# Performance work log

Measured on AMD Instinct MI355X. Metric: run time of the kernel, lower is better.

The kernel has to match this reference:

```python
import jax, jax.numpy as jnp
import numpy as np
import math
from jax import lax

SQRT_HALF = math.sqrt(0.5)

def _causal_dilated_conv(x, w, b, dilation):
    # x: [B, C, T], w: [O, I, K] (torch layout), causal left padding (K-1)*dilation
    k = w.shape[-1]
    pad = (k - 1) * dilation
    y = lax.conv_general_dilated(
        x, w,
        window_strides=(1,),
        padding=((pad, 0),),
        rhs_dilation=(dilation,),
        dimension_numbers=('NCH', 'OIH', 'NCH'),
    )
    return y + b[None, :, None]


def setup_inputs() -> dict:
    key = jax.random.key(0)
    ks = jax.random.split(key, 9)
    B, C, S, T, K = 8, 512, 256, 8192, 2
    scale = 1.0 / np.sqrt(C * K)
    return {
        'x': jax.random.normal(ks[0], (B, C, T), jnp.float32),
        'filter_w': jax.random.normal(ks[1], (C, C, K), jnp.float32) * scale,
        'filter_b': jax.random.normal(ks[2], (C,), jnp.float32) * scale,
        'gate_w': jax.random.normal(ks[3], (C, C, K), jnp.float32) * scale,
        'gate_b': jax.random.normal(ks[4], (C,), jnp.float32) * scale,
        'res_w': jax.random.normal(ks[5], (C, C), jnp.float32) / np.sqrt(C),
        'res_b': jax.random.normal(ks[6], (C,), jnp.float32) / np.sqrt(C),
        'skip_w': jax.random.normal(ks[7], (S, C), jnp.float32) / np.sqrt(C),
        'skip_b': jax.random.normal(ks[8], (S,), jnp.float32) / np.sqrt(C),
        'dilation': 4,
    }


def reference(x, filter_w, filter_b, gate_w, gate_b, res_w, res_b, skip_w, skip_b, dilation):
    filter_out = jnp.tanh(_causal_dilated_conv(x, filter_w, filter_b, dilation))
    gate_out = jax.nn.sigmoid(_causal_dilated_conv(x, gate_w, gate_b, dilation))
    x_gated = filter_out * gate_out  # [B, C, T]
    # 1x1 convs as channel contractions
    res_out = jnp.einsum('oc,bct->bot', res_w, x_gated) + res_b[None, :, None]
    skip_out = jnp.einsum('sc,bct->bst', skip_w, x_gated) + skip_b[None, :, None]
    return ((x + res_out) * SQRT_HALF, skip_out)
```

## Files before the change

### kernel.cpp

```cpp
#include <hip/hip_runtime.h>
#include <hip/hip_bf16.h>

typedef __attribute__((ext_vector_type(4))) float f32x4;
typedef __attribute__((ext_vector_type(8))) short bf16x8;
typedef unsigned int   u32;
typedef unsigned short u16;

#define DPAD 8
#define B_   8
#define C_   512
#define T_   8192
#define S_   256

#define OFF_WBIG 0u
#define OFF_W2   2097152u
#define OFF_B1   2883584u
#define OFF_B2   2887680u
#define OFF_XT   2891776u
#define OFF_ZT   70066176u

__device__ __forceinline__ u16 f2bf(float f) {
  u32 u = __builtin_bit_cast(u32, f);
  u += 0x7FFFu + ((u >> 16) & 1u);
  return (u16)(u >> 16);
}
__device__ __forceinline__ float sigm_(float x) { return 1.0f / (1.0f + __expf(-x)); }
__device__ __forceinline__ float tanh_(float x) { return 2.0f / (1.0f + __expf(-2.0f * x)) - 1.0f; }

__device__ __forceinline__ void gload_lds16(const void* g, void* l) {
  __builtin_amdgcn_global_load_lds(
      (const __attribute__((address_space(1))) void*)g,
      (__attribute__((address_space(3))) void*)l, 16, 0, 0);
}

__global__ void pack_kernel(const float* __restrict__ fw, const float* __restrict__ fb,
                            const float* __restrict__ gw, const float* __restrict__ gb,
                            const float* __restrict__ rw, const float* __restrict__ rb,
                            const float* __restrict__ sw, const float* __restrict__ sb,
                            u16* __restrict__ Wbig, u16* __restrict__ W2,
                            float* __restrict__ b1, float* __restrict__ b2,
                            u16* __restrict__ Xt)
{
  int idx = blockIdx.x * 256 + threadIdx.x;
  if (idx < 1048576) {
    int row = idx >> 10, k = idx & 1023;
    int i = row >> 1;
    const float* src = (row & 1) ? gw : fw;
    float v = src[((i << 9) + (k & 511)) * 2 + ((k < 512) ? 1 : 0)];
    Wbig[idx] = f2bf(v);
    return;
  }
  idx -= 1048576;
  if (idx < 393216) {
    int r = idx >> 9, k = idx & 511;
    float v = (r < 512) ? rw[(r << 9) + k] : sw[((r - 512) << 9) + k];
    W2[idx] = f2bf(v);
    return;
  }
  idx -= 393216;
  if (idx < 1024) { b1[idx] = (idx & 1) ? gb[idx >> 1] : fb[idx >> 1]; return; }
  idx -= 1024;
  if (idx < 768) { b2[idx] = (idx < 512) ? rb[idx] : sb[idx - 512]; return; }
  idx -= 768;
  if (idx < B_ * DPAD * C_) {
    int b = idx >> 12;
    int rest = idx & 4095;
    Xt[(size_t)b * (T_ + DPAD) * C_ + rest] = 0;
  }
}

__global__ __launch_bounds__(256) void transpose_kernel(const float* __restrict__ x,
                                                        u16* __restrict__ Xt)
{
  __shared__ float tile[64][65];
  int bid = blockIdx.x;
  int ct = bid & 7, tt = (bid >> 3) & 127, b = bid >> 10;
  int w = threadIdx.x >> 6, ln = threadIdx.x & 63;
  const float* xp = x + ((size_t)(b * C_ + ct * 64)) * T_ + tt * 64;
#pragma unroll
  for (int r = 0; r < 16; ++r) {
    int cl = r * 4 + w;
    tile[cl][ln] = xp[(size_t)cl * T_ + ln];
  }
  __syncthreads();
  u16* op = Xt + ((size_t)b * (T_ + DPAD) + DPAD + tt * 64) * C_ + ct * 64;
#pragma unroll
  for (int r = 0; r < 16; ++r) {
    int tl = r * 4 + w;
    op[(size_t)tl * C_ + ln] = f2bf(tile[ln][tl]);
  }
}

__global__ __launch_bounds__(512, 2) void gemm1_kernel(
    const u16* __restrict__ W, const u16* __restrict__ Xt,
    const float* __restrict__ b1, u16* __restrict__ Zt,
    const int* __restrict__ dptr)
{
  __shared__ __align__(16) u16 smem[4 * 16384];
  const int dcap = *dptr;
  const int tid = threadIdx.x;
  const int lane = tid & 63, wave = tid >> 6;
  const int wm = wave >> 2, wn = wave & 3;

  const int bid = blockIdx.x;
  const int xcd = bid & 7;
  const int idx = bid >> 3;
  const int mt  = idx & 3;
  const int nt  = (xcd << 5) | (idx >> 2);
  const int m0  = mt * 256;
  const int n0g = nt * 256;
  const int b = n0g >> 13, t0 = n0g & (T_ - 1);

  const int row0 = tid >> 3;
  const int ksw  = (((tid & 7) ^ (row0 & 7)) << 3);
  const size_t xtb = (size_t)b * (T_ + DPAD) * C_;

  f32x4 acc[8][4];
#pragma unroll
  for (int i = 0; i < 8; ++i)
#pragma unroll
    for (int j = 0; j < 4; ++j) acc[i][j] = (f32x4){0.f, 0.f, 0.f, 0.f};

#define STAGE1(kt_, dd) do {                                                   \
    const int kglob_ = (kt_) * 64 + ksw;                                       \
    const int col_ = kglob_ & 511;                                             \
    const int rsh_ = (kglob_ >= 512) ? dcap : 0;                               \
    const u16* gA_ = W + (size_t)(m0 + row0) * 1024 + kglob_;                  \
    const u16* gB_ = Xt + xtb + (size_t)(DPAD + t0 + row0 - rsh_) * C_ + col_; \
    u16* As_ = smem + (dd) * 16384;                                            \
    u16* Bs_ = smem + 32768 + (dd) * 16384;                                    \
    _Pragma("unroll") for (int r_ = 0; r_ < 4; ++r_) {                         \
      gload_lds16(gA_ + (size_t)r_ * 64 * 1024, As_ + r_ * 4096 + tid * 8);    \
      gload_lds16(gB_ + (size_t)r_ * 64 * C_,   Bs_ + r_ * 4096 + tid * 8);    \
    }                                                                          \
  } while (0)

#define COMPUTE1(dd) do {                                                      \
    const u16* Ab_ = smem + (dd) * 16384;                                      \
    const u16* Bb_ = smem + 32768 + (dd) * 16384;                              \
    _Pragma("unroll") for (int s_ = 0; s_ < 2; ++s_) {                         \
      const int blk_ = ((s_ * 4 + (lane >> 4)) ^ (lane & 7)) * 8;              \
      bf16x8 af_[8], bf_[4];                                                   \
      _Pragma("unroll") for (int i_ = 0; i_ < 8; ++i_)                         \
        af_[i_] = *(const bf16x8*)(Ab_ + (wm * 128 + i_ * 16 + (lane & 15)) * 64 + blk_); \
      _Pragma("unroll") for (int j_ = 0; j_ < 4; ++j_)                         \
        bf_[j_] = *(const bf16x8*)(Bb_ + (wn * 64 + j_ * 16 + (lane & 15)) * 64 + blk_);  \
      __builtin_amdgcn_s_setprio(1);                                           \
      _Pragma("unroll") for (int i_ = 0; i_ < 8; ++i_)                         \
        _Pragma("unroll") for (int j_ = 0; j_ < 4; ++j_)                       \
          acc[i_][j_] = __builtin_amdgcn_mfma_f32_16x16x32_bf16(af_[i_], bf_[j_], acc[i_][j_], 0, 0, 0); \
      __builtin_amdgcn_s_setprio(0);                                           \
    }                                                                          \
  } while (0)

  STAGE1(0, 0);
  STAGE1(1, 1);
  for (int it = 0; it < 15; ++it) {
    asm volatile("s_waitcnt vmcnt(8)" ::: "memory");
    __builtin_amdgcn_sched_barrier(0);
    __builtin_amdgcn_s_barrier();
    __builtin_amdgcn_sched_barrier(0);
    COMPUTE1(it & 1);
    __builtin_amdgcn_sched_barrier(0);
    __builtin_amdgcn_s_barrier();
    __builtin_amdgcn_sched_barrier(0);
    if (it < 14) STAGE1(it + 2, it & 1);
  }
  asm volatile("s_waitcnt vmcnt(0)" ::: "memory");
  __builtin_amdgcn_sched_barrier(0);
  __builtin_amdgcn_s_barrier();
  __builtin_amdgcn_sched_barrier(0);
  COMPUTE1(1);

  const int g = lane >> 4, p = lane & 15;
#pragma unroll
  for (int i = 0; i < 8; ++i) {
    const int R = m0 + wm * 128 + i * 16 + (g << 2);
    const float bi0 = b1[R], bi1 = b1[R + 1], bi2 = b1[R + 2], bi3 = b1[R + 3];
    const int c0 = R >> 1;
#pragma unroll
    for (int j = 0; j < 4; ++j) {
      const int ttc = t0 + wn * 64 + j * 16 + p;
      f32x4 v = acc[i][j];
      float z0 = tanh_(v[0] + bi0) * sigm_(v[1] + bi1);
      float z1 = tanh_(v[2] + bi2) * sigm_(v[3] + bi3);
      u32 pk = (u32)f2bf(z0) | ((u32)f2bf(z1) << 16);
      *(u32*)(Zt + (size_t)(b * T_ + ttc) * C_ + c0) = pk;
    }
  }
#undef STAGE1
#undef COMPUTE1
}

__global__ __launch_bounds__(256, 4) void gemm2_kernel(
    const u16* __restrict__ W2, const u16* __restrict__ Zt,
    const float* __restrict__ b2, const float* __restrict__ x,
    float* __restrict__ out)
{
  __shared__ __align__(16) u16 As[128 * 32];
  __shared__ __align__(16) u16 Bs[128 * 32];
  __shared__ __align__(16) float fstall[4 * 1088];
  const int tid = threadIdx.x;
  const int lane = tid & 63, wave = tid >> 6;
  const int wm = wave >> 1, wn = wave & 1;

  const int bid = blockIdx.x;
  const int xcd = bid & 7;
  const int idx = bid >> 3;
  const int mt  = idx % 6;
  const int nt  = (xcd << 6) + idx / 6;
  const int m0 = mt * 128;
  const int n0g = nt * 128;
  const int b = n0g >> 13, t0 = n0g & (T_ - 1);
  const int srow = tid >> 2;
  const int skk  = (tid & 3) * 8;

  f32x4 acc[4][4];
#pragma unroll
  for (int i = 0; i < 4; ++i)
#pragma unroll
    for (int j = 0; j < 4; ++j) acc[i][j] = (f32x4){0.f, 0.f, 0.f, 0.f};

  const int aoff = (wm * 64 + (lane & 15)) * 32 + (lane >> 4) * 8;
  const int boff = (wn * 64 + (lane & 15)) * 32 + (lane >> 4) * 8;
  const size_t ztb = (size_t)b * T_ * C_;

  for (int kc = 0; kc < 16; ++kc) {
    const int k = kc * 32 + skk;
    const u16* gA = W2 + (size_t)(m0 + srow) * 512 + k;
    const u16* gB = Zt + ztb + (size_t)(t0 + srow) * C_ + k;
    gload_lds16(gA,            As + tid * 8);
    gload_lds16(gA + 64 * 512, As + 2048 + tid * 8);
    gload_lds16(gB,            Bs + tid * 8);
    gload_lds16(gB + 64 * C_,  Bs + 2048 + tid * 8);
    asm volatile("s_waitcnt vmcnt(0)" ::: "memory");
    __syncthreads();
    bf16x8 af[4], bfr[4];
#pragma unroll
    for (int i = 0; i < 4; ++i) af[i]  = *(const bf16x8*)(As + aoff + i * 512);
#pragma unroll
    for (int j = 0; j < 4; ++j) bfr[j] = *(const bf16x8*)(Bs + boff + j * 512);
#pragma unroll
    for (int i = 0; i < 4; ++i)
#pragma unroll
      for (int j = 0; j < 4; ++j)
        acc[i][j] = __builtin_amdgcn_mfma_f32_16x16x32_bf16(af[i], bfr[j], acc[i][j], 0, 0, 0);
    __syncthreads();
  }

  float* const fst = fstall + wave * 1088;
  const int g = lane >> 4, p = lane & 15;
  const bool isres = (m0 < 512);

#pragma unroll
  for (int i = 0; i < 4; ++i) {
#pragma unroll
    for (int j = 0; j < 4; ++j)
#pragma unroll
      for (int r = 0; r < 4; ++r)
        fst[(g * 4 + r) * 68 + j * 16 + p] = acc[i][j][r];
#pragma unroll
    for (int q = 0; q < 4; ++q) {
      const int lrow = q * 4 + g;
      const int row = m0 + wm * 64 + i * 16 + lrow;
      const int t = t0 + wn * 64 + p * 4;
      f32x4 v = *(const f32x4*)&fst[lrow * 68 + p * 4];
      const float bias = b2[row];
      f32x4 res;
      if (isres) {
        const size_t o = ((size_t)(b * 512 + row)) * T_ + t;
        f32x4 xv = *(const f32x4*)(x + o);
#pragma unroll
        for (int e = 0; e < 4; ++e)
          res[e] = (xv[e] + v[e] + bias) * 0.70710678118654752f;
        *(f32x4*)(out + o) = res;
      } else {
        const size_t o = (size_t)33554432 + ((size_t)(b * 256 + (row - 512))) * T_ + t;
#pragma unroll
        for (int e = 0; e < 4; ++e)
          res[e] = v[e] + bias;
        *(f32x4*)(out + o) = res;
      }
    }
  }
}

extern "C" void kernel_launch(void* const* d_in, const int* in_sizes, int n_in,
                              void* d_out, int out_size, void* d_ws, size_t ws_size,
                              hipStream_t stream) {
  const float* x  = (const float*)d_in[0];
  const float* fw = (const float*)d_in[1];
  const float* fb = (const float*)d_in[2];
  const float* gw = (const float*)d_in[3];
  const float* gb = (const float*)d_in[4];
  const float* rw = (const float*)d_in[5];
  const float* rb = (const float*)d_in[6];
  const float* sw = (const float*)d_in[7];
  const float* sb = (const float*)d_in[8];
  const int* dil  = (const int*)d_in[9];

  char* ws = (char*)d_ws;
  u16*   Wbig = (u16*)(ws + OFF_WBIG);
  u16*   W2   = (u16*)(ws + OFF_W2);
  float* b1   = (float*)(ws + OFF_B1);
  float* b2   = (float*)(ws + OFF_B2);
  u16*   Xt   = (u16*)(ws + OFF_XT);
  u16*   Zt   = (u16*)(ws + OFF_ZT);
  float* out  = (float*)d_out;

  hipLaunchKernelGGL(pack_kernel, dim3(5767), dim3(256), 0, stream,
                     fw, fb, gw, gb, rw, rb, sw, sb, Wbig, W2, b1, b2, Xt);
  hipLaunchKernelGGL(transpose_kernel, dim3(8192), dim3(256), 0, stream, x, Xt);
  hipLaunchKernelGGL(gemm1_kernel, dim3(1024), dim3(512), 0, stream, Wbig, Xt, b1, Zt, dil);
  hipLaunchKernelGGL(gemm2_kernel, dim3(3072), dim3(256), 0, stream, W2, Zt, b2, x, out);
}
```

Baseline: 317.3 us.

## Split gemm1 main loop into four phases interleaving loads with MFMA

Restructures the gemm1 K-loop from a two-stage-ahead prefetch with two barriers per tile into four phases per tile. Each phase issues a slice of the next tile's global-to-LDS loads alongside a slice of MFMA work, with B fragments held in registers across phases. The aim is to spread memory issue across compute and keep the matrix units fed. In exchange the prefetch depth drops from two tiles to one and there are more barriers, which may expose load latency.

Measured after the change: 307.4 us. 1.03x faster.

```diff
diff --git a/kernel.cpp b/kernel.cpp
--- a/kernel.cpp
+++ b/kernel.cpp
@@ -96,11 +96,12 @@
     const float* __restrict__ b1, u16* __restrict__ Zt,
     const int* __restrict__ dptr)
 {
-  __shared__ __align__(16) u16 smem[4 * 16384];
+  __shared__ __align__(16) u16 smem[65536];
   const int dcap = *dptr;
   const int tid = threadIdx.x;
   const int lane = tid & 63, wave = tid >> 6;
   const int wm = wave >> 2, wn = wave & 3;
+  const int lp = lane & 15, lg = lane >> 4, lx = lane & 7;
 
   const int bid = blockIdx.x;
   const int xcd = bid & 7;
@@ -110,67 +111,80 @@
   const int m0  = mt * 256;
   const int n0g = nt * 256;
   const int b = n0g >> 13, t0 = n0g & (T_ - 1);
-
-  const int row0 = tid >> 3;
-  const int ksw  = (((tid & 7) ^ (row0 & 7)) << 3);
   const size_t xtb = (size_t)b * (T_ + DPAD) * C_;
 
+  const int srl = tid >> 3;
+  const int skb = tid & 7;
+  const int sxk = (skb ^ (srl & 7)) << 3;
+
   f32x4 acc[8][4];
 #pragma unroll
   for (int i = 0; i < 8; ++i)
 #pragma unroll
     for (int j = 0; j < 4; ++j) acc[i][j] = (f32x4){0.f, 0.f, 0.f, 0.f};
 
-#define STAGE1(kt_, dd) do {                                                   \
-    const int kglob_ = (kt_) * 64 + ksw;                                       \
-    const int col_ = kglob_ & 511;                                             \
-    const int rsh_ = (kglob_ >= 512) ? dcap : 0;                               \
-    const u16* gA_ = W + (size_t)(m0 + row0) * 1024 + kglob_;                  \
-    const u16* gB_ = Xt + xtb + (size_t)(DPAD + t0 + row0 - rsh_) * C_ + col_; \
-    u16* As_ = smem + (dd) * 16384;                                            \
-    u16* Bs_ = smem + 32768 + (dd) * 16384;                                    \
-    _Pragma("unroll") for (int r_ = 0; r_ < 4; ++r_) {                         \
-      gload_lds16(gA_ + (size_t)r_ * 64 * 1024, As_ + r_ * 4096 + tid * 8);    \
-      gload_lds16(gB_ + (size_t)r_ * 64 * C_,   Bs_ + r_ * 4096 + tid * 8);    \
-    }                                                                          \
+#define SQA(kt_, dd, q_) do {                                                  \
+    const int row_ = (q_) * 64 + srl;                                          \
+    gload_lds16(W + (size_t)(m0 + row_) * 1024 + (kt_) * 64 + sxk,             \
+                smem + (dd) * 16384 + (q_) * 4096 + tid * 8);                  \
   } while (0)
 
-#define COMPUTE1(dd) do {                                                      \
+#define SQB(kt_, dd, q_) do {                                                  \
+    const int row_ = (q_) * 64 + srl;                                          \
+    const int kg_  = (kt_) * 64 + sxk;                                         \
+    const int rsh_ = (kg_ >= 512) ? dcap : 0;                                  \
+    gload_lds16(Xt + xtb + (size_t)(DPAD + t0 + row_ - rsh_) * C_ + (kg_ & 511), \
+                smem + 32768 + (dd) * 16384 + (q_) * 4096 + tid * 8);          \
+  } while (0)
+
+#define LDA_(Ab_, f_, kk_) \
+  (*(const bf16x8*)((Ab_) + (size_t)(wm * 128 + (f_) * 16 + lp) * 64 + ((((kk_) * 4 + lg) ^ lx) << 3)))
+#define LDB_(Bb_, j_, kk_) \
+  (*(const bf16x8*)((Bb_) + (size_t)(wn * 64 + (j_) * 16 + lp) * 64 + ((((kk_) * 4 + lg) ^ lx) << 3)))
+
+#define PH(dd, p_, WAITS, STAGES) do {                                         \
+    WAITS;                                                                     \
+    __builtin_amdgcn_sched_barrier(0);                                         \
+    __builtin_amdgcn_s_barrier();                                              \
+    __builtin_amdgcn_sched_barrier(0);                                         \
     const u16* Ab_ = smem + (dd) * 16384;                                      \
     const u16* Bb_ = smem + 32768 + (dd) * 16384;                              \
-    _Pragma("unroll") for (int s_ = 0; s_ < 2; ++s_) {                         \
-      const int blk_ = ((s_ * 4 + (lane >> 4)) ^ (lane & 7)) * 8;              \
-      bf16x8 af_[8], bf_[4];                                                   \
-      _Pragma("unroll") for (int i_ = 0; i_ < 8; ++i_)                         \
-        af_[i_] = *(const bf16x8*)(Ab_ + (wm * 128 + i_ * 16 + (lane & 15)) * 64 + blk_); \
-      _Pragma("unroll") for (int j_ = 0; j_ < 4; ++j_)                         \
-        bf_[j_] = *(const bf16x8*)(Bb_ + (wn * 64 + j_ * 16 + (lane & 15)) * 64 + blk_);  \
-      __builtin_amdgcn_s_setprio(1);                                           \
-      _Pragma("unroll") for (int i_ = 0; i_ < 8; ++i_)                         \
-        _Pragma("unroll") for (int j_ = 0; j_ < 4; ++j_)                       \
-          acc[i_][j_] = __builtin_amdgcn_mfma_f32_16x16x32_bf16(af_[i_], bf_[j_], acc[i_][j_], 0, 0, 0); \
-      __builtin_amdgcn_s_setprio(0);                                           \
+    if ((p_) == 0) {                                                           \
+      _Pragma("unroll") for (int j_ = 0; j_ < 4; ++j_) {                       \
+        bfr[j_][0] = LDB_(Bb_, j_, 0); bfr[j_][1] = LDB_(Bb_, j_, 1);          \
+      }                                                                        \
     }                                                                          \
+    bf16x8 a00 = LDA_(Ab_, 2 * (p_), 0),     a01 = LDA_(Ab_, 2 * (p_), 1);     \
+    bf16x8 a10 = LDA_(Ab_, 2 * (p_) + 1, 0), a11 = LDA_(Ab_, 2 * (p_) + 1, 1); \
+    STAGES;                                                                    \
+    __builtin_amdgcn_s_setprio(1);                                             \
+    _Pragma("unroll") for (int j_ = 0; j_ < 4; ++j_) {                         \
+      acc[2*(p_)][j_]   = __builtin_amdgcn_mfma_f32_16x16x32_bf16(a00, bfr[j_][0], acc[2*(p_)][j_],   0, 0, 0); \
+      acc[2*(p_)][j_]   = __builtin_amdgcn_mfma_f32_16x16x32_bf16(a01, bfr[j_][1], acc[2*(p_)][j_],   0, 0, 0); \
+      acc[2*(p_)+1][j_] = __builtin_amdgcn_mfma_f32_16x16x32_bf16(a10, bfr[j_][0], acc[2*(p_)+1][j_], 0, 0, 0); \
+      acc[2*(p_)+1][j_] = __builtin_amdgcn_mfma_f32_16x16x32_bf16(a11, bfr[j_][1], acc[2*(p_)+1][j_], 0, 0, 0); \
+    }                                                                          \
+    __builtin_amdgcn_s_setprio(0);                                             \
   } while (0)
 
-  STAGE1(0, 0);
-  STAGE1(1, 1);
-  for (int it = 0; it < 15; ++it) {
-    asm volatile("s_waitcnt vmcnt(8)" ::: "memory");
-    __builtin_amdgcn_sched_barrier(0);
-    __builtin_amdgcn_s_barrier();
-    __builtin_amdgcn_sched_barrier(0);
-    COMPUTE1(it & 1);
-    __builtin_amdgcn_sched_barrier(0);
-    __builtin_amdgcn_s_barrier();
-    __builtin_amdgcn_sched_barrier(0);
-    if (it < 14) STAGE1(it + 2, it & 1);
-  }
-  asm volatile("s_waitcnt vmcnt(0)" ::: "memory");
-  __builtin_amdgcn_sched_barrier(0);
-  __builtin_amdgcn_s_barrier();
-  __builtin_amdgcn_sched_barrier(0);
-  COMPUTE1(1);
+#define VMW(n_) asm volatile("s_waitcnt vmcnt(" #n_ ")" ::: "memory")
+
+  bf16x8 bfr[4][2];
+
+  SQB(0, 0, 0); SQB(0, 0, 1); SQB(0, 0, 2); SQB(0, 0, 3);
+  SQA(0, 0, 0); SQA(0, 0, 2); SQA(0, 0, 1); SQA(0, 0, 3);
+
+  for (int t = 0; t < 15; ++t) {
+    const int dd = t & 1, de = dd ^ 1;
+    PH(dd, 0, VMW(2), { SQB(t + 1, de, 0); SQB(t + 1, de, 1); });
+    PH(dd, 1,       , { SQB(t + 1, de, 2); SQB(t + 1, de, 3); });
+    PH(dd, 2, VMW(4), { SQA(t + 1, de, 0); SQA(t + 1, de, 2); });
+    PH(dd, 3,       , { SQA(t + 1, de, 1); SQA(t + 1, de, 3); });
+  }
+  PH(1, 0, VMW(2), );
+  PH(1, 1,       , );
+  PH(1, 2, VMW(0), );
+  PH(1, 3,       , );
 
   const int g = lane >> 4, p = lane & 15;
 #pragma unroll
@@ -188,8 +202,12 @@
       *(u32*)(Zt + (size_t)(b * T_ + ttc) * C_ + c0) = pk;
     }
   }
-#undef STAGE1
-#undef COMPUTE1
+#undef SQA
+#undef SQB
+#undef LDA_
+#undef LDB_
+#undef PH
+#undef VMW
 }
 
 __global__ __launch_bounds__(256, 4) void gemm2_kernel(
```

## Replace LDS-staged gemm1 mainloop with direct global-to-register double-buffered loads

Applied to the files above, without the earlier changes.

The gemm1 kernel no longer stages A and B tiles through shared memory with async global-to-LDS loads and barriers. Each wave now loads its MFMA fragments directly from global memory into registers, double-buffered across 32-wide k steps. This removes the LDS traffic and workgroup barriers. In exchange, tiles shared across waves are fetched redundantly from global or L2, loads are less coalesced, and register pressure rises, which can hurt occupancy.

Result: slower. 544.5 us (+71.6%).

```diff
diff --git a/kernel.cpp b/kernel.cpp
--- a/kernel.cpp
+++ b/kernel.cpp
@@ -96,11 +96,11 @@
     const float* __restrict__ b1, u16* __restrict__ Zt,
     const int* __restrict__ dptr)
 {
-  __shared__ __align__(16) u16 smem[4 * 16384];
   const int dcap = *dptr;
   const int tid = threadIdx.x;
   const int lane = tid & 63, wave = tid >> 6;
   const int wm = wave >> 2, wn = wave & 3;
+  const int lp = lane & 15, lg = lane >> 4;
 
   const int bid = blockIdx.x;
   const int xcd = bid & 7;
@@ -110,9 +110,6 @@
   const int m0  = mt * 256;
   const int n0g = nt * 256;
   const int b = n0g >> 13, t0 = n0g & (T_ - 1);
-
-  const int row0 = tid >> 3;
-  const int ksw  = (((tid & 7) ^ (row0 & 7)) << 3);
   const size_t xtb = (size_t)b * (T_ + DPAD) * C_;
 
   f32x4 acc[8][4];
@@ -121,61 +118,40 @@
 #pragma unroll
     for (int j = 0; j < 4; ++j) acc[i][j] = (f32x4){0.f, 0.f, 0.f, 0.f};
 
-#define STAGE1(kt_, dd) do {                                                   \
-    const int kglob_ = (kt_) * 64 + ksw;                                       \
-    const int col_ = kglob_ & 511;                                             \
-    const int rsh_ = (kglob_ >= 512) ? dcap : 0;                               \
-    const u16* gA_ = W + (size_t)(m0 + row0) * 1024 + kglob_;                  \
-    const u16* gB_ = Xt + xtb + (size_t)(DPAD + t0 + row0 - rsh_) * C_ + col_; \
-    u16* As_ = smem + (dd) * 16384;                                            \
-    u16* Bs_ = smem + 32768 + (dd) * 16384;                                    \
-    _Pragma("unroll") for (int r_ = 0; r_ < 4; ++r_) {                         \
-      gload_lds16(gA_ + (size_t)r_ * 64 * 1024, As_ + r_ * 4096 + tid * 8);    \
-      gload_lds16(gB_ + (size_t)r_ * 64 * C_,   Bs_ + r_ * 4096 + tid * 8);    \
-    }                                                                          \
+  const u16* const aBase = W + (size_t)(m0 + wm * 128 + lp) * 1024 + lg * 8;
+  const u16* const bBase = Xt + xtb + (size_t)(DPAD + t0 + wn * 64 + lp) * C_ + lg * 8;
+
+#define LOADS(g_, Ab, Bb) do {                                                 \
+    const int kk_  = (g_) * 32;                                                \
+    const int col_ = kk_ & 511;                                                \
+    const int rsh_ = (kk_ >= 512) ? dcap : 0;                                  \
+    const u16* pa_ = aBase + kk_;                                              \
+    const u16* pb_ = bBase + col_ - (size_t)rsh_ * C_;                         \
+    _Pragma("unroll") for (int i_ = 0; i_ < 8; ++i_)                           \
+      Ab[i_] = *(const bf16x8*)(pa_ + (size_t)i_ * 16 * 1024);                 \
+    _Pragma("unroll") for (int j_ = 0; j_ < 4; ++j_)                           \
+      Bb[j_] = *(const bf16x8*)(pb_ + (size_t)j_ * 16 * C_);                   \
   } while (0)
 
-#define COMPUTE1(dd) do {                                                      \
-    const u16* Ab_ = smem + (dd) * 16384;                                      \
-    const u16* Bb_ = smem + 32768 + (dd) * 16384;                              \
-    _Pragma("unroll") for (int s_ = 0; s_ < 2; ++s_) {                         \
-      const int blk_ = ((s_ * 4 + (lane >> 4)) ^ (lane & 7)) * 8;              \
-      bf16x8 af_[8], bf_[4];                                                   \
-      _Pragma("unroll") for (int i_ = 0; i_ < 8; ++i_)                         \
-        af_[i_] = *(const bf16x8*)(Ab_ + (wm * 128 + i_ * 16 + (lane & 15)) * 64 + blk_); \
+#define MM(Ab, Bb) do {                                                        \
+    _Pragma("unroll") for (int i_ = 0; i_ < 8; ++i_)                           \
       _Pragma("unroll") for (int j_ = 0; j_ < 4; ++j_)                         \
-        bf_[j_] = *(const bf16x8*)(Bb_ + (wn * 64 + j_ * 16 + (lane & 15)) * 64 + blk_);  \
-      __builtin_amdgcn_s_setprio(1);                                           \
-      _Pragma("unroll") for (int i_ = 0; i_ < 8; ++i_)                         \
-        _Pragma("unroll") for (int j_ = 0; j_ < 4; ++j_)                       \
-          acc[i_][j_] = __builtin_amdgcn_mfma_f32_16x16x32_bf16(af_[i_], bf_[j_], acc[i_][j_], 0, 0, 0); \
-      __builtin_amdgcn_s_setprio(0);                                           \
-    }                                                                          \
+        acc[i_][j_] = __builtin_amdgcn_mfma_f32_16x16x32_bf16(Ab[i_], Bb[j_], acc[i_][j_], 0, 0, 0); \
   } while (0)
 
-  STAGE1(0, 0);
-  STAGE1(1, 1);
-  for (int it = 0; it < 15; ++it) {
-    asm volatile("s_waitcnt vmcnt(8)" ::: "memory");
-    __builtin_amdgcn_sched_barrier(0);
-    __builtin_amdgcn_s_barrier();
-    __builtin_amdgcn_sched_barrier(0);
-    COMPUTE1(it & 1);
-    __builtin_amdgcn_sched_barrier(0);
-    __builtin_amdgcn_s_barrier();
-    __builtin_amdgcn_sched_barrier(0);
-    if (it < 14) STAGE1(it + 2, it & 1);
-  }
-  asm volatile("s_waitcnt vmcnt(0)" ::: "memory");
-  __builtin_amdgcn_sched_barrier(0);
-  __builtin_amdgcn_s_barrier();
-  __builtin_amdgcn_sched_barrier(0);
-  COMPUTE1(1);
-
-  const int g = lane >> 4, p = lane & 15;
+  bf16x8 A0[8], B0[4], A1[8], B1[4];
+  LOADS(0, A0, B0);
+#pragma unroll 2
+  for (int g = 0; g < 31; ++g) {
+    if (g & 1) { LOADS(g + 1, A0, B0); } else { LOADS(g + 1, A1, B1); }
+    if (g & 1) { MM(A1, B1); } else { MM(A0, B0); }
+  }
+  MM(A1, B1);
+
+  const int g4 = lane >> 4, p = lane & 15;
 #pragma unroll
   for (int i = 0; i < 8; ++i) {
-    const int R = m0 + wm * 128 + i * 16 + (g << 2);
+    const int R = m0 + wm * 128 + i * 16 + (g4 << 2);
     const float bi0 = b1[R], bi1 = b1[R + 1], bi2 = b1[R + 2], bi3 = b1[R + 3];
     const int c0 = R >> 1;
 #pragma unroll
@@ -188,8 +164,8 @@
       *(u32*)(Zt + (size_t)(b * T_ + ttc) * C_ + c0) = pk;
     }
   }
-#undef STAGE1
-#undef COMPUTE1
+#undef LOADS
+#undef MM
 }
 
 __global__ __launch_bounds__(256, 4) void gemm2_kernel(
```
